# Kernel optimization log

Hardware: AMD Instinct MI355X
Metric: run time of the kernel (lower is better)

## Reference

```python
import jax, jax.numpy as jnp
import numpy as np

N_STATES = 12
N_SUBJECTS = 100
N_CHANNELS = 64
BATCH = 32
SEQ = 1024
LAMBDA_MU = 1.0
LAMBDA_L = 1.0


def _make_chol(key, shape):
    # valid lower-triangular Cholesky factors with positive diagonal
    a = jax.random.normal(key, shape, dtype=jnp.float32) * 0.05
    eye = jnp.eye(shape[-1], dtype=jnp.float32)
    return jnp.tril(a) + eye


def setup_inputs() -> dict:
    key = jax.random.key(0)
    ks = jax.random.split(key, 7)
    data = jax.random.normal(ks[0], (BATCH, SEQ, N_CHANNELS), dtype=jnp.float32)
    mu_pop = jax.random.normal(ks[1], (N_STATES, N_CHANNELS), dtype=jnp.float32)
    L_pop = _make_chol(ks[2], (N_STATES, N_CHANNELS, N_CHANNELS))
    mu_subj = jax.random.normal(ks[3], (N_SUBJECTS, N_STATES, N_CHANNELS), dtype=jnp.float32)
    L_subj = _make_chol(ks[4], (N_SUBJECTS, N_STATES, N_CHANNELS, N_CHANNELS))
    gamma = jax.random.uniform(ks[5], (BATCH, SEQ, N_STATES), dtype=jnp.float32)
    gamma = gamma / jnp.sum(gamma, axis=-1, keepdims=True)  # responsibilities sum to 1
    subject_ids = jax.random.randint(ks[6], (BATCH, 1), 0, N_SUBJECTS, dtype=jnp.int32)
    return {"data": data, "mu_pop": mu_pop, "L_pop": L_pop,
            "mu_subj": mu_subj, "L_subj": L_subj, "gamma": gamma,
            "subject_ids": subject_ids}


def reference(data, mu_pop, L_pop, mu_subj, L_subj, gamma, subject_ids):
    sid = subject_ids.reshape(-1).astype(jnp.int32)            # (B,)
    mu_b = mu_subj[sid]                                        # (B,K,C)
    L_b = L_subj[sid]                                          # (B,K,C,C)

    C = data.shape[-1]
    # diff[b,k,c,t] = data[b,t,c] - mu_b[b,k,c]  -> (B,K,C,T)
    diff = jnp.transpose(data, (0, 2, 1))[:, None, :, :] - mu_b[:, :, :, None]
    # batched triangular solve: z = L^{-1} diff  (B,K,C,T)
    z = jax.lax.linalg.triangular_solve(L_b, diff, left_side=True, lower=True)
    quad = jnp.sum(z * z, axis=2)                              # (B,K,T)
    logdet = jnp.sum(jnp.log(jnp.diagonal(L_b, axis1=-2, axis2=-1)), axis=-1)  # (B,K)
    log_2pi = jnp.float32(np.log(2.0 * np.pi))
    log_probs = -0.5 * quad - logdet[:, :, None] - 0.5 * C * log_2pi  # (B,K,T)

    weighted_ll = jnp.einsum('btk,bkt->bt', gamma, log_probs)  # (B,T)
    # calculation == 'sum': sum over time, mean over batch
    ll = jnp.mean(jnp.sum(weighted_ll, axis=1))
    nll = -ll

    n_total = jnp.float32(mu_subj.shape[0])
    present = jnp.zeros((mu_subj.shape[0],), dtype=jnp.float32).at[sid].set(1.0)
    mu_reg = jnp.sum(present * jnp.sum((mu_subj - mu_pop[None]) ** 2, axis=(1, 2)))
    L_reg = jnp.sum(present * jnp.sum((L_subj - L_pop[None]) ** 2, axis=(1, 2, 3)))
    scale = jnp.sum(present) / n_total
    reg = (LAMBDA_MU / 2.0 * mu_reg + LAMBDA_L / 2.0 * L_reg) * scale

    total = nll + reg
    return total[None]  # shape (1,), matching tf.expand_dims(total_loss, -1)
```

## Files before the change

### kernel.cpp

```cpp
#include <hip/hip_runtime.h>
#include <math.h>

#define NB 32
#define NT 1024
#define NK 12
#define NC 64
#define NS 100
#define SOLVE_BLOCKS (NB * NK * 4)
#define REG_BLOCKS (NS * NK)

typedef __attribute__((ext_vector_type(8))) short short8v;
typedef __attribute__((ext_vector_type(4))) float f32x4;


__device__ __forceinline__ short f2bf(float f) {
  union { float f; unsigned u; } v{f};
  unsigned r = v.u + 0x7fffu + ((v.u >> 16) & 1u);
  return (short)(r >> 16);
}

__global__ __launch_bounds__(128) void init_kernel(int* __restrict__ present) {
  int tid = threadIdx.x;
  if (tid < NS) present[tid] = 0;
}

template <int C>
struct Row {
  static __device__ __forceinline__ void run(float (&z)[NC],
                                             const float4* __restrict__ Ls4,
                                             float& quad) {
    float a0 = z[C];
    float a1 = 0.0f;
    float diag = 0.0f;
#pragma unroll
    for (int g = 0; g <= C / 4; ++g) {
      float4 v = Ls4[C * 16 + g];
#pragma unroll
      for (int e = 0; e < 4; ++e) {
        int j = 4 * g + e;
        float ve = (e == 0) ? v.x : (e == 1) ? v.y : (e == 2) ? v.z : v.w;
        if (j < C) {
          if (j & 1)
            a1 = fmaf(-ve, z[j], a1);
          else
            a0 = fmaf(-ve, z[j], a0);
        } else if (j == C) {
          diag = ve;
        }
      }
    }
    float zc = (a0 + a1) * __builtin_amdgcn_rcpf(diag);
    z[C] = zc;
    quad = fmaf(zc, zc, quad);
    Row<C + 1>::run(z, Ls4, quad);
  }
};
template <>
struct Row<NC> {
  static __device__ __forceinline__ void run(float (&)[NC], const float4*,
                                             float&) {}
};

__global__ __launch_bounds__(64) void invert_kernel(
    const float* __restrict__ L_subj, const int* __restrict__ sids,
    unsigned short* __restrict__ Wws) {
  int b = blockIdx.x / NK;
  int k = blockIdx.x % NK;
  int j = threadIdx.x;
  int sid = __builtin_amdgcn_readfirstlane(sids[b]);

  __shared__ float4 Ls4[NC * NC / 4];
  const float4* Lg =
      reinterpret_cast<const float4*>(L_subj + (size_t)(sid * NK + k) * NC * NC);
#pragma unroll
  for (int i = 0; i < 16; ++i) Ls4[j + 64 * i] = Lg[j + 64 * i];
  __syncthreads();

  float z[NC];
#pragma unroll
  for (int c = 0; c < NC; ++c) z[c] = (c == j) ? 1.0f : 0.0f;
  float dummy = 0.0f;
  Row<0>::run(z, Ls4, dummy);

  __shared__ float Wlds[NC * (NC + 1)];
#pragma unroll
  for (int r = 0; r < NC; ++r) Wlds[r * (NC + 1) + j] = z[r];
  __syncthreads();

  const float* wr = Wlds + j * (NC + 1);
  unsigned* dst =
      reinterpret_cast<unsigned*>(Wws + (size_t)(b * NK + k) * NC * NC) + j * 32;
#pragma unroll
  for (int i = 0; i < 32; ++i) {
    unsigned lo = (unsigned short)f2bf(wr[2 * i]);
    unsigned hi = (unsigned short)f2bf(wr[2 * i + 1]);
    dst[i] = lo | (hi << 16);
  }
}

__global__ __launch_bounds__(64) void mfma_kernel(
    const float* __restrict__ data,
    const float* __restrict__ mu_subj,
    const float* __restrict__ L_subj,
    const float* __restrict__ gamma,
    const int*   __restrict__ sids,
    const unsigned short* __restrict__ Wws,
    float* __restrict__ solve_part,
    int*   __restrict__ present) {
  int blk = blockIdx.x;
  int x   = blk & 7;
  int r   = blk >> 3;
  int b   = (r / 48) * 8 + x;
  int rem = r % 48;
  int k   = rem >> 2;
  int q   = rem & 3;
  int lane = threadIdx.x;
  int g = lane >> 4;
  int m = lane & 15;

  int sid = __builtin_amdgcn_readfirstlane(sids[b]);
  if (lane == 0 && k == 0 && q == 0) present[sid] = 1;

  const float* Lb = L_subj + (size_t)(sid * NK + k) * NC * NC;
  float ld = __logf(Lb[lane * (NC + 1)]);
#pragma unroll
  for (int off = 1; off < 64; off <<= 1) ld += __shfl_xor(ld, off);

  const unsigned short* Wp = Wws + (size_t)(b * NK + k) * NC * NC;
  short8v afrag[4][2];
#pragma unroll
  for (int ct = 0; ct < 4; ++ct)
#pragma unroll
    for (int kk = 0; kk < 2; ++kk)
      afrag[ct][kk] = *reinterpret_cast<const short8v*>(
          Wp + (ct * 16 + m) * NC + kk * 32 + g * 8);

  const float* mu = mu_subj + (size_t)(sid * NK + k) * NC;
  float4 mu0a = *reinterpret_cast<const float4*>(mu + g * 8);
  float4 mu0b = *reinterpret_cast<const float4*>(mu + g * 8 + 4);
  float4 mu1a = *reinterpret_cast<const float4*>(mu + 32 + g * 8);
  float4 mu1b = *reinterpret_cast<const float4*>(mu + 32 + g * 8 + 4);

  float wacc = 0.0f;
  int t0 = q * 256;
#pragma unroll 2
  for (int tt = 0; tt < 16; ++tt) {
    int t = t0 + tt * 16 + m;
    const float* dp = data + ((size_t)(b * NT + t)) * NC;

    short8v bf0, bf1;
    {
      const float4* dv = reinterpret_cast<const float4*>(dp + g * 8);
      float4 v0 = dv[0], v1 = dv[1];
      bf0[0] = f2bf(v0.x - mu0a.x);
      bf0[1] = f2bf(v0.y - mu0a.y);
      bf0[2] = f2bf(v0.z - mu0a.z);
      bf0[3] = f2bf(v0.w - mu0a.w);
      bf0[4] = f2bf(v1.x - mu0b.x);
      bf0[5] = f2bf(v1.y - mu0b.y);
      bf0[6] = f2bf(v1.z - mu0b.z);
      bf0[7] = f2bf(v1.w - mu0b.w);
    }
    {
      const float4* dv = reinterpret_cast<const float4*>(dp + 32 + g * 8);
      float4 v0 = dv[0], v1 = dv[1];
      bf1[0] = f2bf(v0.x - mu1a.x);
      bf1[1] = f2bf(v0.y - mu1a.y);
      bf1[2] = f2bf(v0.z - mu1a.z);
      bf1[3] = f2bf(v0.w - mu1a.w);
      bf1[4] = f2bf(v1.x - mu1b.x);
      bf1[5] = f2bf(v1.y - mu1b.y);
      bf1[6] = f2bf(v1.z - mu1b.z);
      bf1[7] = f2bf(v1.w - mu1b.w);
    }

    f32x4 acc0 = {0.f, 0.f, 0.f, 0.f}, acc1 = acc0, acc2 = acc0, acc3 = acc0;
    acc0 = __builtin_amdgcn_mfma_f32_16x16x32_bf16(afrag[0][0], bf0, acc0, 0, 0, 0);
    acc0 = __builtin_amdgcn_mfma_f32_16x16x32_bf16(afrag[0][1], bf1, acc0, 0, 0, 0);
    acc1 = __builtin_amdgcn_mfma_f32_16x16x32_bf16(afrag[1][0], bf0, acc1, 0, 0, 0);
    acc1 = __builtin_amdgcn_mfma_f32_16x16x32_bf16(afrag[1][1], bf1, acc1, 0, 0, 0);
    acc2 = __builtin_amdgcn_mfma_f32_16x16x32_bf16(afrag[2][0], bf0, acc2, 0, 0, 0);
    acc2 = __builtin_amdgcn_mfma_f32_16x16x32_bf16(afrag[2][1], bf1, acc2, 0, 0, 0);
    acc3 = __builtin_amdgcn_mfma_f32_16x16x32_bf16(afrag[3][0], bf0, acc3, 0, 0, 0);
    acc3 = __builtin_amdgcn_mfma_f32_16x16x32_bf16(afrag[3][1], bf1, acc3, 0, 0, 0);

    float s = 0.0f;
#pragma unroll
    for (int e = 0; e < 4; ++e) {
      s = fmaf(acc0[e], acc0[e], s);
      s = fmaf(acc1[e], acc1[e], s);
      s = fmaf(acc2[e], acc2[e], s);
      s = fmaf(acc3[e], acc3[e], s);
    }
    s += __shfl_xor(s, 16);
    s += __shfl_xor(s, 32);

    float gam = gamma[((size_t)(b * NT + t)) * NK + k];
    wacc = fmaf(gam, -0.5f * s - ld, wacc);
  }

#pragma unroll
  for (int off = 1; off < 64; off <<= 1) wacc += __shfl_xor(wacc, off);
  if (lane == 0) solve_part[blockIdx.x] = wacc * 0.25f;
}

__global__ __launch_bounds__(256) void reg_kernel(
    const float* __restrict__ mu_pop, const float* __restrict__ L_pop,
    const float* __restrict__ mu_subj, const float* __restrict__ L_subj,
    const int* __restrict__ present, float* __restrict__ mu_part,
    float* __restrict__ L_part) {
  int bid = blockIdx.x;
  int s = bid / NK;
  int k = bid % NK;
  int tid = threadIdx.x;
  if (present[s] == 0) {
    if (tid == 0) {
      mu_part[bid] = 0.0f;
      L_part[bid] = 0.0f;
    }
    return;
  }

  const float4* Ls =
      reinterpret_cast<const float4*>(L_subj + (size_t)(s * NK + k) * NC * NC);
  const float4* Lp =
      reinterpret_cast<const float4*>(L_pop + (size_t)k * NC * NC);
  float sl = 0.0f;
#pragma unroll
  for (int i = 0; i < 4; ++i) {
    int idx = tid + i * 256;
    float4 a = Ls[idx], p = Lp[idx];
    float dx = a.x - p.x, dy = a.y - p.y, dz = a.z - p.z, dw = a.w - p.w;
    sl += dx * dx + dy * dy + dz * dz + dw * dw;
  }
  float sm = 0.0f;
  if (tid < NC) {
    float d = mu_subj[(size_t)(s * NK + k) * NC + tid] - mu_pop[k * NC + tid];
    sm = d * d;
  }
#pragma unroll
  for (int off = 1; off < 64; off <<= 1) {
    sl += __shfl_xor(sl, off);
    sm += __shfl_xor(sm, off);
  }
  __shared__ float rl[4], rm[4];
  int lane = tid & 63;
  if (lane == 0) {
    rl[tid >> 6] = sl;
    rm[tid >> 6] = sm;
  }
  __syncthreads();
  if (tid == 0) {
    mu_part[bid] = rm[0] + rm[1] + rm[2] + rm[3];
    L_part[bid] = rl[0] + rl[1] + rl[2] + rl[3];
  }
}

__global__ __launch_bounds__(256) void finalize_kernel(
    const float* __restrict__ solve_part, const float* __restrict__ mu_part,
    const float* __restrict__ L_part, const int* __restrict__ present,
    float* __restrict__ out) {
  int tid = threadIdx.x;
  double s_ll = 0.0, s_mu = 0.0, s_L = 0.0;
  for (int i = tid; i < SOLVE_BLOCKS; i += 256) s_ll += (double)solve_part[i];
  for (int i = tid; i < REG_BLOCKS; i += 256) {
    s_mu += (double)mu_part[i];
    s_L += (double)L_part[i];
  }
  int cnt = (tid < NS) ? present[tid] : 0;
#pragma unroll
  for (int off = 1; off < 64; off <<= 1) {
    s_ll += __shfl_xor(s_ll, off);
    s_mu += __shfl_xor(s_mu, off);
    s_L += __shfl_xor(s_L, off);
    cnt += __shfl_xor(cnt, off);
  }
  __shared__ double r0[4], r1[4], r2[4];
  __shared__ int r3[4];
  int lane = tid & 63;
  if (lane == 0) {
    r0[tid >> 6] = s_ll;
    r1[tid >> 6] = s_mu;
    r2[tid >> 6] = s_L;
    r3[tid >> 6] = cnt;
  }
  __syncthreads();
  if (tid == 0) {
    double ll_sum = r0[0] + r0[1] + r0[2] + r0[3];
    double mu_reg = r1[0] + r1[1] + r1[2] + r1[3];
    double L_reg = r2[0] + r2[1] + r2[2] + r2[3];
    int c = r3[0] + r3[1] + r3[2] + r3[3];
    double c0 = 0.5 * (double)NC * log(2.0 * M_PI);
    double ll = ll_sum / (double)NB - (double)NT * c0;
    double reg = (0.5 * mu_reg + 0.5 * L_reg) * ((double)c / (double)NS);
    out[0] = (float)(-ll + reg);
  }
}

extern "C" void kernel_launch(void* const* d_in, const int* in_sizes, int n_in,
                              void* d_out, int out_size, void* d_ws,
                              size_t ws_size, hipStream_t stream) {
  const float* data    = (const float*)d_in[0];
  const float* mu_pop  = (const float*)d_in[1];
  const float* L_pop   = (const float*)d_in[2];
  const float* mu_subj = (const float*)d_in[3];
  const float* L_subj  = (const float*)d_in[4];
  const float* gamma   = (const float*)d_in[5];
  const int*   sids    = (const int*)d_in[6];
  float* out = (float*)d_out;

  unsigned short* Wws = (unsigned short*)d_ws;
  float* solve_part = (float*)((char*)d_ws + (size_t)NB * NK * NC * NC * 2);
  float* mu_part    = solve_part + SOLVE_BLOCKS;
  float* L_part     = mu_part + REG_BLOCKS;
  int*   present    = (int*)(L_part + REG_BLOCKS);

  hipLaunchKernelGGL(init_kernel, dim3(1), dim3(128), 0, stream, present);
  hipLaunchKernelGGL(invert_kernel, dim3(NB * NK), dim3(64), 0, stream,
                     L_subj, sids, Wws);
  hipLaunchKernelGGL(mfma_kernel, dim3(SOLVE_BLOCKS), dim3(64), 0, stream,
                     data, mu_subj, L_subj, gamma, sids, Wws, solve_part,
                     present);
  hipLaunchKernelGGL(reg_kernel, dim3(REG_BLOCKS), dim3(256), 0, stream,
                     mu_pop, L_pop, mu_subj, L_subj, present, mu_part, L_part);
  hipLaunchKernelGGL(finalize_kernel, dim3(1), dim3(256), 0, stream,
                     solve_part, mu_part, L_part, present, out);
}
```

Measured before the change: 44.91 us.

## Fuse inversion and regularizer into one prep kernel, drop present array, split time finer

Merges the L-inverse kernel and the regularizer kernel into a single 256-thread prep launch. Presence is computed by ballot over the subject ids, which removes the init kernel and the present buffer. The log-determinant is computed once per (b,k) in prep instead of in every MFMA block. The MFMA kernel splits time into 8 chunks per (b,k) with a fully unrolled loop, prefetches gamma, uses the packed bf16 conversion intrinsic, and drops the per-step cross-lane shuffles. This cuts launch count and redundant work but leaves three of the four waves idle during the triangular inversion, and it doubles the MFMA grid.

```diff
diff --git a/kernel.cpp b/kernel.cpp
--- a/kernel.cpp
+++ b/kernel.cpp
@@ -1,4 +1,5 @@
 #include <hip/hip_runtime.h>
+#include <hip/hip_bf16.h>
 #include <math.h>
 
 #define NB 32
@@ -6,22 +7,20 @@
 #define NK 12
 #define NC 64
 #define NS 100
-#define SOLVE_BLOCKS (NB * NK * 4)
+#define INV_BLOCKS (NB * NK)
 #define REG_BLOCKS (NS * NK)
+#define PREP_BLOCKS (INV_BLOCKS + REG_BLOCKS)
+#define MFMA_BLOCKS (NB * NK * 8)
 
 typedef __attribute__((ext_vector_type(8))) short short8v;
 typedef __attribute__((ext_vector_type(4))) float f32x4;
 
 
-__device__ __forceinline__ short f2bf(float f) {
-  union { float f; unsigned u; } v{f};
-  unsigned r = v.u + 0x7fffu + ((v.u >> 16) & 1u);
-  return (short)(r >> 16);
-}
-
-__global__ __launch_bounds__(128) void init_kernel(int* __restrict__ present) {
-  int tid = threadIdx.x;
-  if (tid < NS) present[tid] = 0;
+__device__ __forceinline__ unsigned pk2(float a, float b) {
+  float2 f2{a, b};
+  __hip_bfloat162 h = __float22bfloat162_rn(f2);
+  union { __hip_bfloat162 h; unsigned u; } c{h};
+  return c.u;
 }
 
 template <int C>
@@ -61,70 +60,129 @@
                                              float&) {}
 };
 
-__global__ __launch_bounds__(64) void invert_kernel(
-    const float* __restrict__ L_subj, const int* __restrict__ sids,
-    unsigned short* __restrict__ Wws) {
-  int b = blockIdx.x / NK;
-  int k = blockIdx.x % NK;
-  int j = threadIdx.x;
-  int sid = __builtin_amdgcn_readfirstlane(sids[b]);
-
-  __shared__ float4 Ls4[NC * NC / 4];
-  const float4* Lg =
-      reinterpret_cast<const float4*>(L_subj + (size_t)(sid * NK + k) * NC * NC);
-#pragma unroll
-  for (int i = 0; i < 16; ++i) Ls4[j + 64 * i] = Lg[j + 64 * i];
+__global__ __launch_bounds__(256) void prep_kernel(
+    const float* __restrict__ mu_pop, const float* __restrict__ L_pop,
+    const float* __restrict__ mu_subj, const float* __restrict__ L_subj,
+    const int* __restrict__ sids, unsigned short* __restrict__ Wws,
+    float* __restrict__ ldws, float* __restrict__ mu_part,
+    float* __restrict__ L_part) {
+  __shared__ float smem[NC * (NC + 1)];
+  int bid = blockIdx.x;
+  int tid = threadIdx.x;
+
+  if (bid < INV_BLOCKS) {
+    int b = bid / NK, k = bid % NK;
+    int sid = __builtin_amdgcn_readfirstlane(sids[b]);
+    const float4* Lg =
+        reinterpret_cast<const float4*>(L_subj + (size_t)(sid * NK + k) * NC * NC);
+    float4* Ls4 = reinterpret_cast<float4*>(smem);
+#pragma unroll
+    for (int i = 0; i < 4; ++i) Ls4[tid + 256 * i] = Lg[tid + 256 * i];
+    __syncthreads();
+
+    int j = tid & 63;
+    int wv = tid >> 6;
+    float z[NC];
+    float ld = 0.0f;
+    if (wv == 0) {
+      ld = __logf(smem[j * (NC + 1)]);
+#pragma unroll
+      for (int off = 1; off < 64; off <<= 1) ld += __shfl_xor(ld, off);
+#pragma unroll
+      for (int c = 0; c < NC; ++c) z[c] = (c == j) ? 1.0f : 0.0f;
+      float dummy = 0.0f;
+      Row<0>::run(z, reinterpret_cast<const float4*>(smem), dummy);
+    }
+    __syncthreads();
+    if (wv == 0) {
+#pragma unroll
+      for (int rr = 0; rr < NC; ++rr) smem[rr * (NC + 1) + j] = z[rr];
+      if (j == 0) ldws[bid] = ld;
+    }
+    __syncthreads();
+    unsigned* dst = reinterpret_cast<unsigned*>(Wws + (size_t)bid * NC * NC);
+#pragma unroll
+    for (int i = 0; i < 8; ++i) {
+      int flat = i * 256 + tid;
+      int rr = flat >> 5;
+      int c2 = flat & 31;
+      dst[flat] = pk2(smem[rr * (NC + 1) + 2 * c2], smem[rr * (NC + 1) + 2 * c2 + 1]);
+    }
+    return;
+  }
+
+  int rb = bid - INV_BLOCKS;
+  int s = rb / NK, k = rb % NK;
+  int lane = tid & 63;
+  int sv = sids[lane & 31];
+  bool pres = __ballot(sv == s) != 0ull;
+  if (!pres) {
+    if (tid == 0) {
+      mu_part[rb] = 0.0f;
+      L_part[rb] = 0.0f;
+    }
+    return;
+  }
+
+  const float4* Ls =
+      reinterpret_cast<const float4*>(L_subj + (size_t)(s * NK + k) * NC * NC);
+  const float4* Lp = reinterpret_cast<const float4*>(L_pop + (size_t)k * NC * NC);
+  float sl = 0.0f;
+#pragma unroll
+  for (int i = 0; i < 4; ++i) {
+    int idx = tid + i * 256;
+    float4 a = Ls[idx], p = Lp[idx];
+    float dx = a.x - p.x, dy = a.y - p.y, dz = a.z - p.z, dw = a.w - p.w;
+    sl += dx * dx + dy * dy + dz * dz + dw * dw;
+  }
+  float sm = 0.0f;
+  if (tid < NC) {
+    float d = mu_subj[(size_t)(s * NK + k) * NC + tid] - mu_pop[k * NC + tid];
+    sm = d * d;
+  }
+#pragma unroll
+  for (int off = 1; off < 64; off <<= 1) {
+    sl += __shfl_xor(sl, off);
+    sm += __shfl_xor(sm, off);
+  }
+  if (lane == 0) {
+    smem[tid >> 6] = sl;
+    smem[4 + (tid >> 6)] = sm;
+  }
   __syncthreads();
-
-  float z[NC];
-#pragma unroll
-  for (int c = 0; c < NC; ++c) z[c] = (c == j) ? 1.0f : 0.0f;
-  float dummy = 0.0f;
-  Row<0>::run(z, Ls4, dummy);
-
-  __shared__ float Wlds[NC * (NC + 1)];
-#pragma unroll
-  for (int r = 0; r < NC; ++r) Wlds[r * (NC + 1) + j] = z[r];
-  __syncthreads();
-
-  const float* wr = Wlds + j * (NC + 1);
-  unsigned* dst =
-      reinterpret_cast<unsigned*>(Wws + (size_t)(b * NK + k) * NC * NC) + j * 32;
-#pragma unroll
-  for (int i = 0; i < 32; ++i) {
-    unsigned lo = (unsigned short)f2bf(wr[2 * i]);
-    unsigned hi = (unsigned short)f2bf(wr[2 * i + 1]);
-    dst[i] = lo | (hi << 16);
+  if (tid == 0) {
+    mu_part[rb] = smem[4] + smem[5] + smem[6] + smem[7];
+    L_part[rb] = smem[0] + smem[1] + smem[2] + smem[3];
   }
 }
 
 __global__ __launch_bounds__(64) void mfma_kernel(
     const float* __restrict__ data,
     const float* __restrict__ mu_subj,
-    const float* __restrict__ L_subj,
     const float* __restrict__ gamma,
     const int*   __restrict__ sids,
     const unsigned short* __restrict__ Wws,
-    float* __restrict__ solve_part,
-    int*   __restrict__ present) {
+    const float* __restrict__ ldws,
+    float* __restrict__ solve_part) {
   int blk = blockIdx.x;
   int x   = blk & 7;
   int r   = blk >> 3;
-  int b   = (r / 48) * 8 + x;
-  int rem = r % 48;
-  int k   = rem >> 2;
-  int q   = rem & 3;
+  int b   = (r / 96) * 8 + x;
+  int rem = r % 96;
+  int k   = rem >> 3;
+  int q   = rem & 7;
   int lane = threadIdx.x;
   int g = lane >> 4;
   int m = lane & 15;
 
   int sid = __builtin_amdgcn_readfirstlane(sids[b]);
-  if (lane == 0 && k == 0 && q == 0) present[sid] = 1;
-
-  const float* Lb = L_subj + (size_t)(sid * NK + k) * NC * NC;
-  float ld = __logf(Lb[lane * (NC + 1)]);
-#pragma unroll
-  for (int off = 1; off < 64; off <<= 1) ld += __shfl_xor(ld, off);
+  float ld4 = 0.25f * ldws[b * NK + k];
+
+  int t0 = q * 128;
+  float gpre[8];
+#pragma unroll
+  for (int tt = 0; tt < 8; ++tt)
+    gpre[tt] = gamma[((size_t)(b * NT + t0 + tt * 16 + m)) * NK + k];
 
   const unsigned short* Wp = Wws + (size_t)(b * NK + k) * NC * NC;
   short8v afrag[4][2];
@@ -142,47 +200,38 @@
   float4 mu1b = *reinterpret_cast<const float4*>(mu + 32 + g * 8 + 4);
 
   float wacc = 0.0f;
-  int t0 = q * 256;
-#pragma unroll 2
-  for (int tt = 0; tt < 16; ++tt) {
+#pragma unroll
+  for (int tt = 0; tt < 8; ++tt) {
     int t = t0 + tt * 16 + m;
     const float* dp = data + ((size_t)(b * NT + t)) * NC;
 
-    short8v bf0, bf1;
+    union { unsigned u[4]; short8v v; } ub0, ub1;
     {
       const float4* dv = reinterpret_cast<const float4*>(dp + g * 8);
       float4 v0 = dv[0], v1 = dv[1];
-      bf0[0] = f2bf(v0.x - mu0a.x);
-      bf0[1] = f2bf(v0.y - mu0a.y);
-      bf0[2] = f2bf(v0.z - mu0a.z);
-      bf0[3] = f2bf(v0.w - mu0a.w);
-      bf0[4] = f2bf(v1.x - mu0b.x);
-      bf0[5] = f2bf(v1.y - mu0b.y);
-      bf0[6] = f2bf(v1.z - mu0b.z);
-      bf0[7] = f2bf(v1.w - mu0b.w);
+      ub0.u[0] = pk2(v0.x - mu0a.x, v0.y - mu0a.y);
+      ub0.u[1] = pk2(v0.z - mu0a.z, v0.w - mu0a.w);
+      ub0.u[2] = pk2(v1.x - mu0b.x, v1.y - mu0b.y);
+      ub0.u[3] = pk2(v1.z - mu0b.z, v1.w - mu0b.w);
     }
     {
       const float4* dv = reinterpret_cast<const float4*>(dp + 32 + g * 8);
       float4 v0 = dv[0], v1 = dv[1];
-      bf1[0] = f2bf(v0.x - mu1a.x);
-      bf1[1] = f2bf(v0.y - mu1a.y);
-      bf1[2] = f2bf(v0.z - mu1a.z);
-      bf1[3] = f2bf(v0.w - mu1a.w);
-      bf1[4] = f2bf(v1.x - mu1b.x);
-      bf1[5] = f2bf(v1.y - mu1b.y);
-      bf1[6] = f2bf(v1.z - mu1b.z);
-      bf1[7] = f2bf(v1.w - mu1b.w);
+      ub1.u[0] = pk2(v0.x - mu1a.x, v0.y - mu1a.y);
+      ub1.u[1] = pk2(v0.z - mu1a.z, v0.w - mu1a.w);
+      ub1.u[2] = pk2(v1.x - mu1b.x, v1.y - mu1b.y);
+      ub1.u[3] = pk2(v1.z - mu1b.z, v1.w - mu1b.w);
     }
 
     f32x4 acc0 = {0.f, 0.f, 0.f, 0.f}, acc1 = acc0, acc2 = acc0, acc3 = acc0;
-    acc0 = __builtin_amdgcn_mfma_f32_16x16x32_bf16(afrag[0][0], bf0, acc0, 0, 0, 0);
-    acc0 = __builtin_amdgcn_mfma_f32_16x16x32_bf16(afrag[0][1], bf1, acc0, 0, 0, 0);
-    acc1 = __builtin_amdgcn_mfma_f32_16x16x32_bf16(afrag[1][0], bf0, acc1, 0, 0, 0);
-    acc1 = __builtin_amdgcn_mfma_f32_16x16x32_bf16(afrag[1][1], bf1, acc1, 0, 0, 0);
-    acc2 = __builtin_amdgcn_mfma_f32_16x16x32_bf16(afrag[2][0], bf0, acc2, 0, 0, 0);
-    acc2 = __builtin_amdgcn_mfma_f32_16x16x32_bf16(afrag[2][1], bf1, acc2, 0, 0, 0);
-    acc3 = __builtin_amdgcn_mfma_f32_16x16x32_bf16(afrag[3][0], bf0, acc3, 0, 0, 0);
-    acc3 = __builtin_amdgcn_mfma_f32_16x16x32_bf16(afrag[3][1], bf1, acc3, 0, 0, 0);
+    acc0 = __builtin_amdgcn_mfma_f32_16x16x32_bf16(afrag[0][0], ub0.v, acc0, 0, 0, 0);
+    acc0 = __builtin_amdgcn_mfma_f32_16x16x32_bf16(afrag[0][1], ub1.v, acc0, 0, 0, 0);
+    acc1 = __builtin_amdgcn_mfma_f32_16x16x32_bf16(afrag[1][0], ub0.v, acc1, 0, 0, 0);
+    acc1 = __builtin_amdgcn_mfma_f32_16x16x32_bf16(afrag[1][1], ub1.v, acc1, 0, 0, 0);
+    acc2 = __builtin_amdgcn_mfma_f32_16x16x32_bf16(afrag[2][0], ub0.v, acc2, 0, 0, 0);
+    acc2 = __builtin_amdgcn_mfma_f32_16x16x32_bf16(afrag[2][1], ub1.v, acc2, 0, 0, 0);
+    acc3 = __builtin_amdgcn_mfma_f32_16x16x32_bf16(afrag[3][0], ub0.v, acc3, 0, 0, 0);
+    acc3 = __builtin_amdgcn_mfma_f32_16x16x32_bf16(afrag[3][1], ub1.v, acc3, 0, 0, 0);
 
     float s = 0.0f;
 #pragma unroll
@@ -192,82 +241,36 @@
       s = fmaf(acc2[e], acc2[e], s);
       s = fmaf(acc3[e], acc3[e], s);
     }
-    s += __shfl_xor(s, 16);
-    s += __shfl_xor(s, 32);
-
-    float gam = gamma[((size_t)(b * NT + t)) * NK + k];
-    wacc = fmaf(gam, -0.5f * s - ld, wacc);
+    wacc = fmaf(gpre[tt], fmaf(-0.5f, s, -ld4), wacc);
   }
 
 #pragma unroll
   for (int off = 1; off < 64; off <<= 1) wacc += __shfl_xor(wacc, off);
-  if (lane == 0) solve_part[blockIdx.x] = wacc * 0.25f;
-}
-
-__global__ __launch_bounds__(256) void reg_kernel(
-    const float* __restrict__ mu_pop, const float* __restrict__ L_pop,
-    const float* __restrict__ mu_subj, const float* __restrict__ L_subj,
-    const int* __restrict__ present, float* __restrict__ mu_part,
-    float* __restrict__ L_part) {
-  int bid = blockIdx.x;
-  int s = bid / NK;
-  int k = bid % NK;
-  int tid = threadIdx.x;
-  if (present[s] == 0) {
-    if (tid == 0) {
-      mu_part[bid] = 0.0f;
-      L_part[bid] = 0.0f;
-    }
-    return;
-  }
-
-  const float4* Ls =
-      reinterpret_cast<const float4*>(L_subj + (size_t)(s * NK + k) * NC * NC);
-  const float4* Lp =
-      reinterpret_cast<const float4*>(L_pop + (size_t)k * NC * NC);
-  float sl = 0.0f;
-#pragma unroll
-  for (int i = 0; i < 4; ++i) {
-    int idx = tid + i * 256;
-    float4 a = Ls[idx], p = Lp[idx];
-    float dx = a.x - p.x, dy = a.y - p.y, dz = a.z - p.z, dw = a.w - p.w;
-    sl += dx * dx + dy * dy + dz * dz + dw * dw;
-  }
-  float sm = 0.0f;
-  if (tid < NC) {
-    float d = mu_subj[(size_t)(s * NK + k) * NC + tid] - mu_pop[k * NC + tid];
-    sm = d * d;
-  }
-#pragma unroll
-  for (int off = 1; off < 64; off <<= 1) {
-    sl += __shfl_xor(sl, off);
-    sm += __shfl_xor(sm, off);
-  }
-  __shared__ float rl[4], rm[4];
-  int lane = tid & 63;
-  if (lane == 0) {
-    rl[tid >> 6] = sl;
-    rm[tid >> 6] = sm;
-  }
-  __syncthreads();
-  if (tid == 0) {
-    mu_part[bid] = rm[0] + rm[1] + rm[2] + rm[3];
-    L_part[bid] = rl[0] + rl[1] + rl[2] + rl[3];
-  }
+  if (lane == 0) solve_part[blockIdx.x] = wacc;
 }
 
 __global__ __launch_bounds__(256) void finalize_kernel(
     const float* __restrict__ solve_part, const float* __restrict__ mu_part,
-    const float* __restrict__ L_part, const int* __restrict__ present,
+    const float* __restrict__ L_part, const int* __restrict__ sids,
     float* __restrict__ out) {
+  __shared__ int ssv[32];
+  __shared__ double r0[4], r1[4], r2[4];
+  __shared__ int r3[4];
   int tid = threadIdx.x;
+  if (tid < 32) ssv[tid] = sids[tid];
+  __syncthreads();
+
   double s_ll = 0.0, s_mu = 0.0, s_L = 0.0;
-  for (int i = tid; i < SOLVE_BLOCKS; i += 256) s_ll += (double)solve_part[i];
+  for (int i = tid; i < MFMA_BLOCKS; i += 256) s_ll += (double)solve_part[i];
   for (int i = tid; i < REG_BLOCKS; i += 256) {
     s_mu += (double)mu_part[i];
     s_L += (double)L_part[i];
   }
-  int cnt = (tid < NS) ? present[tid] : 0;
+  int cnt = 0;
+  if (tid < NS) {
+    for (int i = 0; i < 32; ++i)
+      if (ssv[i] == tid) { cnt = 1; break; }
+  }
 #pragma unroll
   for (int off = 1; off < 64; off <<= 1) {
     s_ll += __shfl_xor(s_ll, off);
@@ -275,8 +278,6 @@
     s_L += __shfl_xor(s_L, off);
     cnt += __shfl_xor(cnt, off);
   }
-  __shared__ double r0[4], r1[4], r2[4];
-  __shared__ int r3[4];
   int lane = tid & 63;
   if (lane == 0) {
     r0[tid >> 6] = s_ll;
@@ -310,19 +311,16 @@
   float* out = (float*)d_out;
 
   unsigned short* Wws = (unsigned short*)d_ws;
-  float* solve_part = (float*)((char*)d_ws + (size_t)NB * NK * NC * NC * 2);
-  float* mu_part    = solve_part + SOLVE_BLOCKS;
+  float* ldws       = (float*)((char*)d_ws + (size_t)INV_BLOCKS * NC * NC * 2);
+  float* solve_part = ldws + INV_BLOCKS;
+  float* mu_part    = solve_part + MFMA_BLOCKS;
   float* L_part     = mu_part + REG_BLOCKS;
-  int*   present    = (int*)(L_part + REG_BLOCKS);
-
-  hipLaunchKernelGGL(init_kernel, dim3(1), dim3(128), 0, stream, present);
-  hipLaunchKernelGGL(invert_kernel, dim3(NB * NK), dim3(64), 0, stream,
-                     L_subj, sids, Wws);
-  hipLaunchKernelGGL(mfma_kernel, dim3(SOLVE_BLOCKS), dim3(64), 0, stream,
-                     data, mu_subj, L_subj, gamma, sids, Wws, solve_part,
-                     present);
-  hipLaunchKernelGGL(reg_kernel, dim3(REG_BLOCKS), dim3(256), 0, stream,
-                     mu_pop, L_pop, mu_subj, L_subj, present, mu_part, L_part);
+
+  hipLaunchKernelGGL(prep_kernel, dim3(PREP_BLOCKS), dim3(256), 0, stream,
+                     mu_pop, L_pop, mu_subj, L_subj, sids, Wws, ldws, mu_part,
+                     L_part);
+  hipLaunchKernelGGL(mfma_kernel, dim3(MFMA_BLOCKS), dim3(64), 0, stream,
+                     data, mu_subj, gamma, sids, Wws, ldws, solve_part);
   hipLaunchKernelGGL(finalize_kernel, dim3(1), dim3(256), 0, stream,
-                     solve_part, mu_part, L_part, present, out);
-}
+                     solve_part, mu_part, L_part, sids, out);
+}
```

New measurement: 43.05 us (median of 2 runs). 4.2% less time.
